# Optimization experiments

Measured on AMD Instinct MI355X. Metric: run time of the kernel, lower is better.

Reference implementation:

```python
import jax, jax.numpy as jnp
import numpy as np

B, C = 16, 256          # batch, feature_dim
P, K = 20, 50           # max_polygons, max_points
H4 = W4 = 32            # p4 spatial
H2 = W2 = 128           # p2 spatial


def setup_inputs() -> dict:
    key = jax.random.key(0)
    ks = jax.random.split(key, 12)

    def w(k, shape, fan_in):
        return jax.random.normal(k, shape, jnp.float32) * (1.0 / np.sqrt(fan_in))

    return {
        "p4": jax.random.normal(ks[0], (B, C, H4, W4), jnp.float32),
        "p2": jax.random.normal(ks[1], (B, C, H2, W2), jnp.float32),
        "segmentation": jax.random.uniform(ks[2], (B, 1, H2, W2), dtype=jnp.float32),
        # init_net linears (torch layout: [out, in])
        "W1": w(ks[3], (1024, C * 64), C * 64), "b1": jnp.zeros((1024,), jnp.float32),
        "W2": w(ks[4], (P * K * 2, 1024), 1024), "b2": jnp.zeros((P * K * 2,), jnp.float32),
        # refine_net
        "R1": w(ks[5], (128, C + 2), C + 2), "rb1": jnp.zeros((128,), jnp.float32),
        "R2": w(ks[6], (64, 128), 128), "rb2": jnp.zeros((64,), jnp.float32),
        "R3": w(ks[7], (2, 64), 64), "rb3": jnp.zeros((2,), jnp.float32),
        # validity_net
        "V1": w(ks[8], (128, K * 2), K * 2), "vb1": jnp.zeros((128,), jnp.float32),
        "V2": w(ks[9], (1, 128), 128), "vb2": jnp.zeros((1,), jnp.float32),
    }


def _bilinear_sample(img, xy):
    """F.grid_sample(align_corners=False, padding='zeros') for one image.
    img: [C, H, W]; xy: [N, 2] in [-1, 1] with xy[:, 0]=x (width), xy[:, 1]=y (height).
    Returns [N, C]."""
    Cc, H, W = img.shape
    x = ((xy[:, 0] + 1.0) * W - 1.0) * 0.5
    y = ((xy[:, 1] + 1.0) * H - 1.0) * 0.5
    x0 = jnp.floor(x)
    y0 = jnp.floor(y)
    wx1 = x - x0
    wy1 = y - y0

    def corner(xi, yi, wgt):
        valid = (xi >= 0) & (xi <= W - 1) & (yi >= 0) & (yi <= H - 1)
        xc = jnp.clip(xi, 0, W - 1).astype(jnp.int32)
        yc = jnp.clip(yi, 0, H - 1).astype(jnp.int32)
        v = img[:, yc, xc]  # [C, N]
        return v * (wgt * valid.astype(img.dtype))[None, :]

    out = (corner(x0, y0, (1 - wx1) * (1 - wy1))
           + corner(x0 + 1, y0, wx1 * (1 - wy1))
           + corner(x0, y0 + 1, (1 - wx1) * wy1)
           + corner(x0 + 1, y0 + 1, wx1 * wy1))
    return out.T  # [N, C]


def reference(p4, p2, segmentation, W1, b1, W2, b2, R1, rb1, R2, rb2, R3, rb3, V1, vb1, V2, vb2):
    Bn, Cc, h4, w4 = p4.shape
    pooled = p4.reshape(Bn, Cc, 8, h4 // 8, 8, w4 // 8).mean(axis=(3, 5))
    flat = pooled.reshape(Bn, -1)                       # [B, C*64]
    h = jax.nn.relu(flat @ W1.T + b1)
    init_pts = jax.nn.sigmoid(h @ W2.T + b2).reshape(Bn, P, K, 2)

    # refine: grid_sample point gather + 3-layer MLP
    grid = init_pts * 2.0 - 1.0                          # [B, P, K, 2]
    xy = grid.reshape(Bn, -1, 2)                         # [B, N=P*K, 2]
    sampled = jax.vmap(_bilinear_sample)(p2, xy)         # [B, N, C]
    coords = init_pts.reshape(Bn, -1, 2)
    feat = jnp.concatenate([sampled, coords], axis=-1)   # [B, N, C+2]
    h1 = jax.nn.relu(feat @ R1.T + rb1)
    h2 = jax.nn.relu(h1 @ R2.T + rb2)
    disp = jnp.tanh(h2 @ R3.T + rb3).reshape(Bn, P, K, 2)
    refined = jnp.clip(init_pts + 0.1 * disp, 0.0, 1.0)

    # validity
    pf = refined.reshape(Bn * P, K * 2)
    v = jax.nn.sigmoid(jax.nn.relu(pf @ V1.T + vb1) @ V2.T + vb2).reshape(Bn, P)
    return refined, v, init_pts
```

## Files before the change

### kernel.cpp

```cpp
#include <hip/hip_runtime.h>
#include <hip/hip_bf16.h>
#include <math.h>

#define NB 16
#define NC 256
#define NPTS 1000
#define NN2 2000
#define D1 1024
#define KFLAT 16384

typedef unsigned short ushort8 __attribute__((ext_vector_type(8)));

static __device__ __forceinline__ float bf2f(unsigned short v) {
    union { unsigned int u; float f; } x;
    x.u = ((unsigned int)v) << 16;
    return x.f;
}

__global__ __launch_bounds__(256) void k_poolprep(const float* __restrict__ p4,
                                                  const float* __restrict__ R1,
                                                  const float* __restrict__ V1,
                                                  __hip_bfloat16* __restrict__ flat_bf,
                                                  float* __restrict__ R1t,
                                                  float* __restrict__ V1t_g) {
    int idx = blockIdx.x * 256 + threadIdx.x;
    if (idx < 262144) {
        int bc = idx >> 6;
        int ij = idx & 63;
        int i = ij >> 3, j = ij & 7;
        const float* src = p4 + ((size_t)bc * 32 + i * 4) * 32 + j * 4;
        float s = 0.f;
#pragma unroll
        for (int di = 0; di < 4; ++di) {
            float4 v = *reinterpret_cast<const float4*>(src + di * 32);
            s += v.x + v.y + v.z + v.w;
        }
        flat_bf[idx] = __float2bfloat16(s * (1.0f / 16.0f));
    } else {
        int t = idx - 262144;
        if (t < 33024) {
            int j = t / 258, k = t % 258;
            R1t[k * 128 + j] = R1[t];
        } else if (t < 33024 + 12800) {
            int t2 = t - 33024;
            int j = t2 / 100, k = t2 % 100;
            V1t_g[k * 128 + j] = V1[t2];
        }
    }
}

__global__ __launch_bounds__(512) void k_fc1(const __hip_bfloat16* __restrict__ flat_bf,
                                             const float* __restrict__ W1,
                                             const float* __restrict__ b1,
                                             float* __restrict__ h) {
    __shared__ unsigned short tile[2 * 16 * 512];
    __shared__ float red[8 * 16];
    const int tid = threadIdx.x;
    const int wave = tid >> 6, lane = tid & 63;
    const int colw = wave & 3, half = wave >> 2;
    const int n = blockIdx.x * 4 + colw;
    float acc[16];
#pragma unroll
    for (int m = 0; m < 16; ++m) acc[m] = 0.f;
    const float4* W1r4 = reinterpret_cast<const float4*>(W1 + (size_t)n * KFLAT + half * 8192);
    const ushort8* flat8 = reinterpret_cast<const ushort8*>(flat_bf);
    ushort8* tile8 = reinterpret_cast<ushort8*>(tile);

    float4 wa = W1r4[lane * 2], wb = W1r4[lane * 2 + 1];
    for (int it = 0; it < 16; ++it) {
        __syncthreads();
#pragma unroll
        for (int r = 0; r < 4; ++r) {
            int idx = tid + r * 512;
            int hh = idx >> 10, m = (idx >> 6) & 15, off = idx & 63;
            tile8[idx] = flat8[m * 2048 + hh * 1024 + it * 64 + off];
        }
        __syncthreads();
        float4 na = wa, nb = wb;
        if (it < 15) {
            na = W1r4[(it + 1) * 128 + lane * 2];
            nb = W1r4[(it + 1) * 128 + lane * 2 + 1];
        }
#pragma unroll
        for (int m = 0; m < 16; ++m) {
            ushort8 u = tile8[half * 1024 + m * 64 + lane];
            float s = wa.x * bf2f(u.s0) + wa.y * bf2f(u.s1)
                    + wa.z * bf2f(u.s2) + wa.w * bf2f(u.s3)
                    + wb.x * bf2f(u.s4) + wb.y * bf2f(u.s5)
                    + wb.z * bf2f(u.s6) + wb.w * bf2f(u.s7);
            acc[m] += s;
        }
        wa = na; wb = nb;
    }
#pragma unroll
    for (int m = 0; m < 16; ++m) {
        float v = acc[m];
#pragma unroll
        for (int off = 32; off > 0; off >>= 1) v += __shfl_xor(v, off, 64);
        acc[m] = v;
    }
    __syncthreads();
    if (lane == 0) {
#pragma unroll
        for (int m = 0; m < 16; ++m) red[wave * 16 + m] = acc[m];
    }
    __syncthreads();
    if (tid < 64) {
        int c = tid >> 4, m = tid & 15;
        float v = red[c * 16 + m] + red[(c + 4) * 16 + m] + b1[blockIdx.x * 4 + c];
        h[m * D1 + blockIdx.x * 4 + c] = fmaxf(v, 0.f);
    }
}

__global__ __launch_bounds__(256) void k_fc2(const float* __restrict__ h,
                                             const float* __restrict__ W2,
                                             const float* __restrict__ b2,
                                             float* __restrict__ init_ws,
                                             float* __restrict__ out_init) {
    const int tid = threadIdx.x;
    const int wave = tid >> 6, lane = tid & 63;
    const int n = blockIdx.x * 4 + wave;
    float acc[16];
#pragma unroll
    for (int m = 0; m < 16; ++m) acc[m] = 0.f;
    const float4* W2r = reinterpret_cast<const float4*>(W2 + (size_t)n * D1);
    const float4* h4  = reinterpret_cast<const float4*>(h);
#pragma unroll
    for (int it = 0; it < 4; ++it) {
        int k4 = it * 64 + lane;
        float4 w = W2r[k4];
#pragma unroll
        for (int m = 0; m < 16; ++m) {
            float4 f = h4[m * 256 + k4];
            acc[m] += w.x * f.x + w.y * f.y + w.z * f.z + w.w * f.w;
        }
    }
    float bias = b2[n];
#pragma unroll
    for (int m = 0; m < 16; ++m) {
        float v = acc[m];
#pragma unroll
        for (int off = 32; off > 0; off >>= 1) v += __shfl_xor(v, off, 64);
        if (lane == 0) {
            float s = 1.f / (1.f + expf(-(v + bias)));
            init_ws[m * NN2 + n] = s;
            out_init[m * NN2 + n] = s;
        }
    }
}

__global__ __launch_bounds__(1024) void k_sample(const float* __restrict__ p2,
                                                 const float* __restrict__ init_ws,
                                                 __hip_bfloat16* __restrict__ sampled) {
    __shared__ float img[128 * 128];
    const int bc = blockIdx.x;
    const int b = bc >> 8;
    const float4* src4 = reinterpret_cast<const float4*>(p2 + (size_t)bc * 16384);
    float4* dst4 = reinterpret_cast<float4*>(img);
#pragma unroll
    for (int i = 0; i < 4; ++i)
        dst4[threadIdx.x + i * 1024] = src4[threadIdx.x + i * 1024];
    __syncthreads();
    const float* ip = init_ws + b * NN2;
    const int n = threadIdx.x;
    if (n < NPTS) {
        float2 sxy = *reinterpret_cast<const float2*>(ip + 2 * n);
        float x = sxy.x * 128.f - 0.5f;
        float y = sxy.y * 128.f - 0.5f;
        float x0f = floorf(x), y0f = floorf(y);
        float wx = x - x0f, wy = y - y0f;
        int x0 = (int)x0f, y0 = (int)y0f;
        int x1 = x0 + 1, y1 = y0 + 1;
        bool vx0 = (x0 >= 0) && (x0 <= 127);
        bool vx1 = (x1 >= 0) && (x1 <= 127);
        bool vy0 = (y0 >= 0) && (y0 <= 127);
        bool vy1 = (y1 >= 0) && (y1 <= 127);
        int cx0 = min(max(x0, 0), 127), cx1 = min(max(x1, 0), 127);
        int cy0 = min(max(y0, 0), 127), cy1 = min(max(y1, 0), 127);
        float v00 = (vx0 && vy0) ? img[cy0 * 128 + cx0] : 0.f;
        float v10 = (vx1 && vy0) ? img[cy0 * 128 + cx1] : 0.f;
        float v01 = (vx0 && vy1) ? img[cy1 * 128 + cx0] : 0.f;
        float v11 = (vx1 && vy1) ? img[cy1 * 128 + cx1] : 0.f;
        float r = v00 * (1.f - wx) * (1.f - wy) + v10 * wx * (1.f - wy)
                + v01 * (1.f - wx) * wy + v11 * wx * wy;
        sampled[(size_t)bc * NPTS + n] = __float2bfloat16(r);
    }
}

__global__ __launch_bounds__(256) void k_refine(const __hip_bfloat16* __restrict__ sampled,
                                                const float* __restrict__ init_ws,
                                                const float* __restrict__ R1t,
                                                const float* __restrict__ rb1,
                                                const float* __restrict__ R2,
                                                const float* __restrict__ rb2,
                                                const float* __restrict__ R3,
                                                const float* __restrict__ rb3,
                                                float* __restrict__ refined) {
    __shared__ float smem[12288];
    const int tid = threadIdx.x;
    const int b = blockIdx.x >> 4;
    const int n0 = (blockIdx.x & 15) * 64;
    const int jt = tid >> 4;
    const int nt = tid & 15;
    float acc[8][4];
#pragma unroll
    for (int a = 0; a < 8; ++a)
#pragma unroll
        for (int c = 0; c < 4; ++c) acc[a][c] = 0.f;

    const float4* R1t4 = reinterpret_cast<const float4*>(R1t);
    float4* As4 = reinterpret_cast<float4*>(smem);

    for (int k0 = 0; k0 < 256; k0 += 64) {
        __syncthreads();
#pragma unroll
        for (int i = 0; i < 8; ++i) {
            int idx4 = tid + i * 256;
            As4[idx4] = R1t4[k0 * 32 + idx4];
        }
#pragma unroll
        for (int c2 = 0; c2 < 2; ++c2) {
            int chunk = tid + c2 * 256;
            int row = chunk >> 3, off = chunk & 7;
            int nb = n0 + off * 8;
            float4 f0 = make_float4(0.f, 0.f, 0.f, 0.f);
            float4 f1 = make_float4(0.f, 0.f, 0.f, 0.f);
            if (nb + 8 <= NPTS) {
                ushort8 u = *reinterpret_cast<const ushort8*>(
                    reinterpret_cast<const unsigned short*>(sampled)
                    + ((size_t)(b * 256 + k0 + row)) * NPTS + nb);
                f0 = make_float4(bf2f(u.s0), bf2f(u.s1), bf2f(u.s2), bf2f(u.s3));
                f1 = make_float4(bf2f(u.s4), bf2f(u.s5), bf2f(u.s6), bf2f(u.s7));
            }
            float* bp = &smem[8192 + row * 64 + off * 8];
            *reinterpret_cast<float4*>(bp) = f0;
            *reinterpret_cast<float4*>(bp + 4) = f1;
        }
        __syncthreads();
#pragma unroll 4
        for (int kk = 0; kk < 64; ++kk) {
            const float* Ar = &smem[kk * 128];
            const float* Br = &smem[8192 + kk * 64];
            float4 a0 = *reinterpret_cast<const float4*>(Ar + jt * 4);
            float4 a1 = *reinterpret_cast<const float4*>(Ar + 64 + jt * 4);
            float4 bb = *reinterpret_cast<const float4*>(Br + nt * 4);
            float av[8] = {a0.x, a0.y, a0.z, a0.w, a1.x, a1.y, a1.z, a1.w};
            float bv[4] = {bb.x, bb.y, bb.z, bb.w};
#pragma unroll
            for (int a = 0; a < 8; ++a)
#pragma unroll
                for (int c = 0; c < 4; ++c)
                    acc[a][c] = fmaf(av[a], bv[c], acc[a][c]);
        }
    }
    const int nbase = n0 + nt * 4;
    float4 cA = *reinterpret_cast<const float4*>(init_ws + b * NN2 + 2 * nbase);
    float4 cB = *reinterpret_cast<const float4*>(init_ws + b * NN2 + 2 * nbase + 4);
    __syncthreads();
#pragma unroll
    for (int a = 0; a < 8; ++a) {
        int j = (a < 4) ? (jt * 4 + a) : (64 + jt * 4 + (a - 4));
        float rx = R1t[256 * 128 + j];
        float ry = R1t[257 * 128 + j];
        float bj = rb1[j];
        float4 hv;
        hv.x = fmaxf(acc[a][0] + rx * cA.x + ry * cA.y + bj, 0.f);
        hv.y = fmaxf(acc[a][1] + rx * cA.z + ry * cA.w + bj, 0.f);
        hv.z = fmaxf(acc[a][2] + rx * cB.x + ry * cB.y + bj, 0.f);
        hv.w = fmaxf(acc[a][3] + rx * cB.z + ry * cB.w + bj, 0.f);
        *reinterpret_cast<float4*>(&smem[j * 64 + nt * 4]) = hv;
    }
    __syncthreads();
    const int wave = tid >> 6, lane = tid & 63;
    const int jb = __builtin_amdgcn_readfirstlane(wave * 16);
    float a2[16];
#pragma unroll
    for (int jj = 0; jj < 16; ++jj) a2[jj] = rb2[jb + jj];
#pragma unroll 4
    for (int k = 0; k < 128; ++k) {
        float hv = smem[k * 64 + lane];
#pragma unroll
        for (int jj = 0; jj < 16; ++jj)
            a2[jj] = fmaf(R2[(jb + jj) * 128 + k], hv, a2[jj]);
    }
    float d0 = 0.f, d1 = 0.f;
#pragma unroll
    for (int jj = 0; jj < 16; ++jj) {
        float a = fmaxf(a2[jj], 0.f);
        d0 = fmaf(R3[jb + jj], a, d0);
        d1 = fmaf(R3[64 + jb + jj], a, d1);
    }
    float* part = &smem[8192];
    part[(wave * 2 + 0) * 64 + lane] = d0;
    part[(wave * 2 + 1) * 64 + lane] = d1;
    __syncthreads();
    if (tid < 64) {
        float s0 = 0.f, s1 = 0.f;
#pragma unroll
        for (int w = 0; w < 4; ++w) {
            s0 += part[(w * 2 + 0) * 64 + tid];
            s1 += part[(w * 2 + 1) * 64 + tid];
        }
        int n = n0 + tid;
        int nc = min(n, NPTS - 1);
        float2 ip = *reinterpret_cast<const float2*>(init_ws + b * NN2 + 2 * nc);
        float rx = fminf(fmaxf(ip.x + 0.1f * tanhf(s0 + rb3[0]), 0.f), 1.f);
        float ry = fminf(fmaxf(ip.y + 0.1f * tanhf(s1 + rb3[1]), 0.f), 1.f);
        if (n < NPTS) {
            *reinterpret_cast<float2*>(refined + ((size_t)b * NPTS + n) * 2)
                = make_float2(rx, ry);
        }
    }
}

__global__ __launch_bounds__(256) void k_vhead(const float* __restrict__ refined,
                                               const float* __restrict__ V1t_g,
                                               const float* __restrict__ vb1,
                                               const float* __restrict__ V2,
                                               const float* __restrict__ vb2,
                                               float* __restrict__ vout) {
    __shared__ float V1t[100][128];
    __shared__ float pf[4][100];
    const int tid = threadIdx.x, wave = tid >> 6, lane = tid & 63;
    for (int idx = tid; idx < 100 * 128; idx += 256)
        V1t[idx >> 7][idx & 127] = V1t_g[idx];
    __syncthreads();
    const int row = blockIdx.x * 4 + wave;
    const float* src = refined + row * 100;
    if (lane < 50) {
        pf[wave][lane] = src[lane];
        pf[wave][lane + 50] = src[lane + 50];
    }
    __syncthreads();
    float a0 = vb1[lane], a1 = vb1[64 + lane];
#pragma unroll 10
    for (int k = 0; k < 100; ++k) {
        float p = pf[wave][k];
        a0 += V1t[k][lane] * p;
        a1 += V1t[k][64 + lane] * p;
    }
    float s = fmaxf(a0, 0.f) * V2[lane] + fmaxf(a1, 0.f) * V2[64 + lane];
#pragma unroll
    for (int off = 32; off > 0; off >>= 1) s += __shfl_xor(s, off, 64);
    if (lane == 0) vout[row] = 1.f / (1.f + expf(-(s + vb2[0])));
}

extern "C" void kernel_launch(void* const* d_in, const int* in_sizes, int n_in,
                              void* d_out, int out_size, void* d_ws, size_t ws_size,
                              hipStream_t stream) {
    const float* p4  = (const float*)d_in[0];
    const float* p2  = (const float*)d_in[1];
    const float* W1  = (const float*)d_in[3];
    const float* b1  = (const float*)d_in[4];
    const float* W2  = (const float*)d_in[5];
    const float* b2  = (const float*)d_in[6];
    const float* R1  = (const float*)d_in[7];
    const float* rb1 = (const float*)d_in[8];
    const float* R2  = (const float*)d_in[9];
    const float* rb2 = (const float*)d_in[10];
    const float* R3  = (const float*)d_in[11];
    const float* rb3 = (const float*)d_in[12];
    const float* V1  = (const float*)d_in[13];
    const float* vb1 = (const float*)d_in[14];
    const float* V2  = (const float*)d_in[15];
    const float* vb2 = (const float*)d_in[16];
    float* out = (float*)d_out;

    char* ws = (char*)d_ws;
    __hip_bfloat16* flat_bf = (__hip_bfloat16*)(ws + 0);
    float* h    = (float*)(ws + 524288);
    float* ipts = (float*)(ws + 589824);
    __hip_bfloat16* samp = (__hip_bfloat16*)(ws + 717824);
    float* R1t  = (float*)(ws + 8909824);
    float* V1t_g= (float*)(ws + 9041920);

    k_poolprep<<<1204, 256, 0, stream>>>(p4, R1, V1, flat_bf, R1t, V1t_g);
    k_fc1<<<256, 512, 0, stream>>>(flat_bf, W1, b1, h);
    k_fc2<<<500, 256, 0, stream>>>(h, W2, b2, ipts, out + 32320);
    k_sample<<<4096, 1024, 0, stream>>>(p2, ipts, samp);
    k_refine<<<256, 256, 0, stream>>>(samp, ipts, R1t, rb1, R2, rb2, R3, rb3, out);
    k_vhead<<<80, 256, 0, stream>>>(out, V1t_g, vb1, V2, vb2, out + 32000);
}
```

Measured before the change: 510.7 us.

## Use direct global-to-LDS loads in sampler and restructure refine MLP across 512 threads

The sampler kernel now stages each 128x128 p2 channel into LDS with global_load_lds builtins instead of going through registers. The refine kernel loads the entire 256x64 sampled tile into shared memory once and computes layer 1 with per-wave scalar weight reads from R1t, replacing the register-tiled A/B GEMM. It also doubles the block size to 512 so each wave handles fewer outputs in layer 2. The aim is to cut register staging and per-chunk synchronisations. The cost is that R1t now comes from global/scalar memory on every k step, and the larger LDS footprint lowers occupancy.

```diff
diff --git a/kernel.cpp b/kernel.cpp
--- a/kernel.cpp
+++ b/kernel.cpp
@@ -10,6 +10,8 @@
 #define KFLAT 16384
 
 typedef unsigned short ushort8 __attribute__((ext_vector_type(8)));
+typedef unsigned int uint_as1 __attribute__((address_space(1)));
+typedef unsigned int uint_as3 __attribute__((address_space(3)));
 
 static __device__ __forceinline__ float bf2f(unsigned short v) {
     union { unsigned int u; float f; } x;
@@ -156,10 +158,14 @@
     const int bc = blockIdx.x;
     const int b = bc >> 8;
     const float4* src4 = reinterpret_cast<const float4*>(p2 + (size_t)bc * 16384);
-    float4* dst4 = reinterpret_cast<float4*>(img);
-#pragma unroll
-    for (int i = 0; i < 4; ++i)
-        dst4[threadIdx.x + i * 1024] = src4[threadIdx.x + i * 1024];
+    const int wv = threadIdx.x >> 6, ln = threadIdx.x & 63;
+#pragma unroll
+    for (int i = 0; i < 4; ++i) {
+        int base = i * 1024 + wv * 64;
+        __builtin_amdgcn_global_load_lds(
+            (const uint_as1*)(src4 + base + ln),
+            (uint_as3*)(img + base * 4), 16, 0, 0);
+    }
     __syncthreads();
     const float* ip = init_ws + b * NN2;
     const int n = threadIdx.x;
@@ -187,7 +193,7 @@
     }
 }
 
-__global__ __launch_bounds__(256) void k_refine(const __hip_bfloat16* __restrict__ sampled,
+__global__ __launch_bounds__(512) void k_refine(const __hip_bfloat16* __restrict__ sampled,
                                                 const float* __restrict__ init_ws,
                                                 const float* __restrict__ R1t,
                                                 const float* __restrict__ rb1,
@@ -196,99 +202,74 @@
                                                 const float* __restrict__ R3,
                                                 const float* __restrict__ rb3,
                                                 float* __restrict__ refined) {
-    __shared__ float smem[12288];
+    __shared__ float smem[16384];
     const int tid = threadIdx.x;
+    const int wave = tid >> 6, lane = tid & 63;
     const int b = blockIdx.x >> 4;
     const int n0 = (blockIdx.x & 15) * 64;
-    const int jt = tid >> 4;
-    const int nt = tid & 15;
-    float acc[8][4];
-#pragma unroll
-    for (int a = 0; a < 8; ++a)
-#pragma unroll
-        for (int c = 0; c < 4; ++c) acc[a][c] = 0.f;
-
-    const float4* R1t4 = reinterpret_cast<const float4*>(R1t);
-    float4* As4 = reinterpret_cast<float4*>(smem);
-
-    for (int k0 = 0; k0 < 256; k0 += 64) {
-        __syncthreads();
-#pragma unroll
-        for (int i = 0; i < 8; ++i) {
-            int idx4 = tid + i * 256;
-            As4[idx4] = R1t4[k0 * 32 + idx4];
-        }
-#pragma unroll
-        for (int c2 = 0; c2 < 2; ++c2) {
-            int chunk = tid + c2 * 256;
-            int row = chunk >> 3, off = chunk & 7;
-            int nb = n0 + off * 8;
-            float4 f0 = make_float4(0.f, 0.f, 0.f, 0.f);
-            float4 f1 = make_float4(0.f, 0.f, 0.f, 0.f);
-            if (nb + 8 <= NPTS) {
-                ushort8 u = *reinterpret_cast<const ushort8*>(
-                    reinterpret_cast<const unsigned short*>(sampled)
-                    + ((size_t)(b * 256 + k0 + row)) * NPTS + nb);
-                f0 = make_float4(bf2f(u.s0), bf2f(u.s1), bf2f(u.s2), bf2f(u.s3));
-                f1 = make_float4(bf2f(u.s4), bf2f(u.s5), bf2f(u.s6), bf2f(u.s7));
-            }
-            float* bp = &smem[8192 + row * 64 + off * 8];
-            *reinterpret_cast<float4*>(bp) = f0;
-            *reinterpret_cast<float4*>(bp + 4) = f1;
-        }
-        __syncthreads();
+
+#pragma unroll
+    for (int c2 = 0; c2 < 4; ++c2) {
+        int chunk = tid + c2 * 512;
+        int row = chunk >> 3, off = chunk & 7;
+        int nb = n0 + off * 8;
+        float4 f0 = make_float4(0.f, 0.f, 0.f, 0.f);
+        float4 f1 = make_float4(0.f, 0.f, 0.f, 0.f);
+        if (nb + 8 <= NPTS) {
+            ushort8 u = *reinterpret_cast<const ushort8*>(
+                reinterpret_cast<const unsigned short*>(sampled)
+                + ((size_t)(b * 256 + row)) * NPTS + nb);
+            f0 = make_float4(bf2f(u.s0), bf2f(u.s1), bf2f(u.s2), bf2f(u.s3));
+            f1 = make_float4(bf2f(u.s4), bf2f(u.s5), bf2f(u.s6), bf2f(u.s7));
+        }
+        float* bp = &smem[row * 64 + off * 8];
+        *reinterpret_cast<float4*>(bp) = f0;
+        *reinterpret_cast<float4*>(bp + 4) = f1;
+    }
+    __syncthreads();
+
+    const int jb = __builtin_amdgcn_readfirstlane(wave * 16);
+    float acc1[16];
+#pragma unroll
+    for (int jj = 0; jj < 16; ++jj) acc1[jj] = 0.f;
 #pragma unroll 4
-        for (int kk = 0; kk < 64; ++kk) {
-            const float* Ar = &smem[kk * 128];
-            const float* Br = &smem[8192 + kk * 64];
-            float4 a0 = *reinterpret_cast<const float4*>(Ar + jt * 4);
-            float4 a1 = *reinterpret_cast<const float4*>(Ar + 64 + jt * 4);
-            float4 bb = *reinterpret_cast<const float4*>(Br + nt * 4);
-            float av[8] = {a0.x, a0.y, a0.z, a0.w, a1.x, a1.y, a1.z, a1.w};
-            float bv[4] = {bb.x, bb.y, bb.z, bb.w};
-#pragma unroll
-            for (int a = 0; a < 8; ++a)
-#pragma unroll
-                for (int c = 0; c < 4; ++c)
-                    acc[a][c] = fmaf(av[a], bv[c], acc[a][c]);
-        }
-    }
-    const int nbase = n0 + nt * 4;
-    float4 cA = *reinterpret_cast<const float4*>(init_ws + b * NN2 + 2 * nbase);
-    float4 cB = *reinterpret_cast<const float4*>(init_ws + b * NN2 + 2 * nbase + 4);
-    __syncthreads();
-#pragma unroll
-    for (int a = 0; a < 8; ++a) {
-        int j = (a < 4) ? (jt * 4 + a) : (64 + jt * 4 + (a - 4));
-        float rx = R1t[256 * 128 + j];
-        float ry = R1t[257 * 128 + j];
-        float bj = rb1[j];
-        float4 hv;
-        hv.x = fmaxf(acc[a][0] + rx * cA.x + ry * cA.y + bj, 0.f);
-        hv.y = fmaxf(acc[a][1] + rx * cA.z + ry * cA.w + bj, 0.f);
-        hv.z = fmaxf(acc[a][2] + rx * cB.x + ry * cB.y + bj, 0.f);
-        hv.w = fmaxf(acc[a][3] + rx * cB.z + ry * cB.w + bj, 0.f);
-        *reinterpret_cast<float4*>(&smem[j * 64 + nt * 4]) = hv;
-    }
-    __syncthreads();
-    const int wave = tid >> 6, lane = tid & 63;
-    const int jb = __builtin_amdgcn_readfirstlane(wave * 16);
-    float a2[16];
-#pragma unroll
-    for (int jj = 0; jj < 16; ++jj) a2[jj] = rb2[jb + jj];
+    for (int kk = 0; kk < 256; ++kk) {
+        float hv = smem[kk * 64 + lane];
+        const float* wr = R1t + kk * 128 + jb;
+#pragma unroll
+        for (int jj = 0; jj < 16; ++jj)
+            acc1[jj] = fmaf(wr[jj], hv, acc1[jj]);
+    }
+    const int n = n0 + lane;
+    const int ncl = min(n, NPTS - 1);
+    float2 cxy = *reinterpret_cast<const float2*>(init_ws + b * NN2 + 2 * ncl);
+    __syncthreads();
+#pragma unroll
+    for (int jj = 0; jj < 16; ++jj) {
+        int j = jb + jj;
+        float hv = fmaxf(acc1[jj] + R1t[256 * 128 + j] * cxy.x
+                                  + R1t[257 * 128 + j] * cxy.y + rb1[j], 0.f);
+        smem[j * 64 + lane] = hv;
+    }
+    __syncthreads();
+
+    const int jb2 = __builtin_amdgcn_readfirstlane(wave * 8);
+    float a2[8];
+#pragma unroll
+    for (int jj = 0; jj < 8; ++jj) a2[jj] = rb2[jb2 + jj];
 #pragma unroll 4
     for (int k = 0; k < 128; ++k) {
         float hv = smem[k * 64 + lane];
 #pragma unroll
-        for (int jj = 0; jj < 16; ++jj)
-            a2[jj] = fmaf(R2[(jb + jj) * 128 + k], hv, a2[jj]);
+        for (int jj = 0; jj < 8; ++jj)
+            a2[jj] = fmaf(R2[(jb2 + jj) * 128 + k], hv, a2[jj]);
     }
     float d0 = 0.f, d1 = 0.f;
 #pragma unroll
-    for (int jj = 0; jj < 16; ++jj) {
+    for (int jj = 0; jj < 8; ++jj) {
         float a = fmaxf(a2[jj], 0.f);
-        d0 = fmaf(R3[jb + jj], a, d0);
-        d1 = fmaf(R3[64 + jb + jj], a, d1);
+        d0 = fmaf(R3[jb2 + jj], a, d0);
+        d1 = fmaf(R3[64 + jb2 + jj], a, d1);
     }
     float* part = &smem[8192];
     part[(wave * 2 + 0) * 64 + lane] = d0;
@@ -297,17 +278,17 @@
     if (tid < 64) {
         float s0 = 0.f, s1 = 0.f;
 #pragma unroll
-        for (int w = 0; w < 4; ++w) {
+        for (int w = 0; w < 8; ++w) {
             s0 += part[(w * 2 + 0) * 64 + tid];
             s1 += part[(w * 2 + 1) * 64 + tid];
         }
-        int n = n0 + tid;
-        int nc = min(n, NPTS - 1);
+        int nn = n0 + tid;
+        int nc = min(nn, NPTS - 1);
         float2 ip = *reinterpret_cast<const float2*>(init_ws + b * NN2 + 2 * nc);
         float rx = fminf(fmaxf(ip.x + 0.1f * tanhf(s0 + rb3[0]), 0.f), 1.f);
         float ry = fminf(fmaxf(ip.y + 0.1f * tanhf(s1 + rb3[1]), 0.f), 1.f);
-        if (n < NPTS) {
-            *reinterpret_cast<float2*>(refined + ((size_t)b * NPTS + n) * 2)
+        if (nn < NPTS) {
+            *reinterpret_cast<float2*>(refined + ((size_t)b * NPTS + nn) * 2)
                 = make_float2(rx, ry);
         }
     }
@@ -378,6 +359,6 @@
     k_fc1<<<256, 512, 0, stream>>>(flat_bf, W1, b1, h);
     k_fc2<<<500, 256, 0, stream>>>(h, W2, b2, ipts, out + 32320);
     k_sample<<<4096, 1024, 0, stream>>>(p2, ipts, samp);
-    k_refine<<<256, 256, 0, stream>>>(samp, ipts, R1t, rb1, R2, rb2, R3, rb3, out);
+    k_refine<<<256, 512, 0, stream>>>(samp, ipts, R1t, rb1, R2, rb2, R3, rb3, out);
     k_vhead<<<80, 256, 0, stream>>>(out, V1t_g, vb1, V2, vb2, out + 32000);
 }
```

Result: no change. 511.5 us (+0.2%).
